# Optimization experiments

Hardware: AMD Instinct MI355X
Metric: run time of the kernel (lower is better)

## Reference

```python
import jax, jax.numpy as jnp
import numpy as np

THRESH = 0.95
SCALE = 20.0
KERNEL = 8  # feature_hw // proto_grid_size = 64 // 8
EPS = 1e-4


def _avg_pool(x, k):
    # x: [b, c, h, w] -> [b, c, h//k, w//k], non-overlapping k x k mean (AvgPool2d(k))
    b, c, h, w = x.shape
    return x.reshape(b, c, h // k, k, w // k, k).mean(axis=(3, 5))


def _safe_norm(x, eps=EPS):
    # L2-normalize along axis 1, clamping the norm at eps (matches safe_norm)
    n = jnp.sqrt(jnp.sum(x * x, axis=1, keepdims=True))
    return x / jnp.maximum(n, eps)


def setup_inputs() -> dict:
    key = jax.random.key(0)
    k1, k2, k3 = jax.random.split(key, 3)
    qry = jax.random.normal(k1, (32, 256, 64, 64), dtype=jnp.float32)
    sup_x = jax.random.normal(k2, (4, 256, 64, 64), dtype=jnp.float32)
    # binary support mask so that (sup_y > 0.95) selects the ones and pooled
    # occupancy exceeds 0.5 for ~half the grid cells -> valid prototypes exist
    sup_y = jax.random.randint(k3, (4, 1, 64, 64), 0, 2).astype(jnp.float32)
    return {"qry": qry, "sup_x": sup_x, "sup_y": sup_y}


def reference(qry, sup_x, sup_y):
    # ---- normalize query features (gridconv mode) ----
    qn = _safe_norm(qry)                                  # [B, C, H, W]

    # ---- prototype extraction (gridconv) ----
    mask_bin = (sup_y > THRESH).astype(qry.dtype)         # [bs, 1, H, W]
    feat_pooled = _avg_pool(sup_x, KERNEL)                # [bs, C, G, G]
    mask_pooled = _avg_pool(mask_bin, KERNEL)             # [bs, 1, G, G]
    valid = (mask_pooled[:, 0] > 0.5).reshape(-1)         # [P] with P = bs*G*G

    C = feat_pooled.shape[1]
    # gather all pooled locations in (image, hi, wi) order, mask out invalid ones
    protos = jnp.transpose(feat_pooled, (0, 2, 3, 1)).reshape(-1, C)  # [P, C]
    protos_n = _safe_norm(protos)                         # [P, C]

    # ---- prediction: conv2d with 1x1 prototype kernels == channel contraction ----
    dists = jnp.einsum('bchw,pc->bphw', qn, protos_n) * SCALE  # [B, P, H, W]
    vmask = valid[None, :, None, None]
    logits = jnp.where(vmask, dists, -jnp.inf)
    w = jax.nn.softmax(logits, axis=1)                    # invalid protos get 0 weight
    pred = jnp.sum(w * jnp.where(vmask, dists, 0.0), axis=1, keepdims=True)  # [B,1,H,W]

    debug_assign = jnp.argmax(logits, axis=1).astype(dists.dtype)  # [B, H, W]
    proto_grid = mask_bin                                 # (sup_y > thresh).float()
    return (pred, debug_assign, proto_grid)
```

## Files before the change

### kernel.cpp

```cpp
#include <hip/hip_runtime.h>
#include <math.h>

constexpr int BQ = 32;
constexpr int C  = 256;
constexpr int HW = 4096;
constexpr int W  = 64;
constexpr int P  = 256;
constexpr float THRESH = 0.95f;
constexpr float SCALE  = 20.0f;
constexpr float EPSF   = 1e-4f;
constexpr double EPSD  = 1e-4;
constexpr float GAP_THRESH = 2e-3f;
constexpr int MAXSUS = 65536;

constexpr int OUT_ASSIGN = BQ * HW;
constexpr int OUT_GRID   = 2 * BQ * HW;

typedef __attribute__((ext_vector_type(8))) short short8;
typedef __attribute__((ext_vector_type(4))) float floatx4;

static __device__ __forceinline__ unsigned short f2bf(float x) {
    unsigned u = __float_as_uint(x);
    u += 0x7FFFu + ((u >> 16) & 1u);
    return (unsigned short)(u >> 16);
}
static __device__ __forceinline__ float bf2f(unsigned short h) {
    return __uint_as_float(((unsigned)h) << 16);
}

#define FRAGOFF(tile, ks, h, lane) (((((tile) * 8 + (ks)) * 2 + (h)) * 64 + (lane)) * 8)

static __device__ __forceinline__ void gl_lds16(const unsigned short* gp, unsigned short* lp) {
    __builtin_amdgcn_global_load_lds(
        (const __attribute__((address_space(1))) unsigned int*)gp,
        (__attribute__((address_space(3))) unsigned int*)lp, 16, 0, 0);
}

__global__ __launch_bounds__(256)
void prep_kernel(const float* __restrict__ sup_x, const float* __restrict__ sup_y,
                 float* __restrict__ out, unsigned short* __restrict__ pB,
                 double* __restrict__ pn64, int* __restrict__ valid,
                 int* __restrict__ counter)
{
    const int p = blockIdx.x;
    const int t = threadIdx.x;
    const int s = p >> 6, gy = (p >> 3) & 7, gx = p & 7;

    const float* base = sup_x + ((size_t)(s * C + t)) * HW + (gy * 8) * W + gx * 8;
    double sum = 0.0;
#pragma unroll
    for (int r = 0; r < 8; ++r) {
        const float4 a  = *(const float4*)(base + r * W);
        const float4 bq = *(const float4*)(base + r * W + 4);
        sum += (double)a.x;  sum += (double)a.y;  sum += (double)a.z;  sum += (double)a.w;
        sum += (double)bq.x; sum += (double)bq.y; sum += (double)bq.z; sum += (double)bq.w;
    }
    const double mean = sum * (1.0 / 64.0);

    __shared__ double red[256];
    red[t] = mean * mean;
    __syncthreads();
    for (int off = 128; off > 0; off >>= 1) {
        if (t < off) red[t] += red[t + off];
        __syncthreads();
    }
    const double nrm = sqrt(red[0]);
    const double pnv = mean / fmax(nrm, EPSD);
    pn64[(size_t)p * C + t] = pnv;

    const float pnf = (float)pnv;
    const unsigned short phi = f2bf(pnf);
    const unsigned short plo = f2bf(pnf - bf2f(phi));
    const int nt = p >> 4, ks = t >> 5, lane = (((t >> 3) & 3) << 4) | (p & 15), j = t & 7;
    pB[FRAGOFF(nt, ks, 0, lane) + j] = phi;
    pB[FRAGOFF(nt, ks, 1, lane) + j] = plo;

    bool mybit = false;
    if (t < 64) {
        const int r = t >> 3, k = t & 7;
        mybit = sup_y[s * HW + (gy * 8 + r) * W + gx * 8 + k] > THRESH;
    }
    const unsigned long long bm = __ballot(mybit);
    if (t == 0) {
        valid[p] = (__popcll(bm) > 32) ? 1 : 0;
        if (p == 0) *counter = 0;
    }
    if (t < 64) {
        const int i = p * 64 + t;
        out[OUT_GRID + i] = (sup_y[i] > THRESH) ? 1.0f : 0.0f;
    }
}

__global__ __launch_bounds__(256, 4)
void dist_kernel(const float* __restrict__ qry, const unsigned short* __restrict__ pB,
                 const int* __restrict__ valid, float* __restrict__ out,
                 int* __restrict__ counter, int* __restrict__ suspects)
{
    __shared__ unsigned short ldsB[16 * 2 * 64 * 8];
    __shared__ int validLds[P];

    const int t    = threadIdx.x;
    const int w    = t >> 6;
    const int l    = t & 63;
    const int quad = l >> 4;
    const int m    = l & 15;

    const int b    = blockIdx.x >> 6;
    const int pos0 = (blockIdx.x & 63) * 64;

    validLds[t] = valid[t];

    const float* qp = qry + (size_t)b * C * HW + pos0 + w * 16 + m;

    floatx4 acc[16];
#pragma unroll
    for (int nt = 0; nt < 16; ++nt) acc[nt] = (floatx4){0.f, 0.f, 0.f, 0.f};

    float vbuf[8];
#pragma unroll
    for (int j = 0; j < 8; ++j)
        vbuf[j] = qp[(size_t)(quad * 8 + j) * HW];

    float ssq = 0.f;
#pragma unroll
    for (int ks = 0; ks < 8; ++ks) {
        __syncthreads();
#pragma unroll
        for (int i = 0; i < 8; ++i) {
            const int idx = w * 8 + i, nt = idx >> 1, h = idx & 1;
            gl_lds16(pB + FRAGOFF(nt, ks, h, 0) + l * 8,
                     &ldsB[(nt * 2 + h) * 512]);
        }
        short8 h8, l8;
#pragma unroll
        for (int j = 0; j < 8; ++j) {
            const float v = vbuf[j];
            ssq = fmaf(v, v, ssq);
            const unsigned short hi = f2bf(v);
            h8[j] = (short)hi;
            l8[j] = (short)f2bf(v - bf2f(hi));
        }
        if (ks < 7) {
#pragma unroll
            for (int j = 0; j < 8; ++j)
                vbuf[j] = qp[(size_t)((ks + 1) * 32 + quad * 8 + j) * HW];
        }
        __syncthreads();
#pragma unroll
        for (int nt = 0; nt < 16; ++nt) {
            const short8 bh = *(const short8*)&ldsB[((nt * 2 + 0) * 64 + l) * 8];
            const short8 bl = *(const short8*)&ldsB[((nt * 2 + 1) * 64 + l) * 8];
            acc[nt] = __builtin_amdgcn_mfma_f32_16x16x32_bf16(h8, bh, acc[nt], 0, 0, 0);
            acc[nt] = __builtin_amdgcn_mfma_f32_16x16x32_bf16(h8, bl, acc[nt], 0, 0, 0);
            acc[nt] = __builtin_amdgcn_mfma_f32_16x16x32_bf16(l8, bh, acc[nt], 0, 0, 0);
        }
    }

    ssq += __shfl_xor(ssq, 16);
    ssq += __shfl_xor(ssq, 32);
    const float scalev = SCALE / fmaxf(sqrtf(ssq), EPSF);

    int vbits = 0;
#pragma unroll
    for (int nt = 0; nt < 16; ++nt) vbits |= validLds[nt * 16 + m] << nt;

    float scr[4];
#pragma unroll
    for (int r = 0; r < 4; ++r) scr[r] = __shfl(scalev, quad * 4 + r);
#pragma unroll
    for (int nt = 0; nt < 16; ++nt)
#pragma unroll
        for (int r = 0; r < 4; ++r) acc[nt][r] *= scr[r];

#pragma unroll
    for (int r = 0; r < 4; ++r) {
        float m1 = -INFINITY, m2 = -INFINITY; int id = 0x7fffffff;
#pragma unroll
        for (int nt = 0; nt < 16; ++nt) {
            if (vbits & (1 << nt)) {
                const float d = acc[nt][r];
                if (d > m1)      { m2 = m1; m1 = d; id = nt * 16 + m; }
                else if (d > m2) { m2 = d; }
            }
        }
#pragma unroll
        for (int sh = 1; sh < 16; sh <<= 1) {
            const float om1 = __shfl_xor(m1, sh);
            const float om2 = __shfl_xor(m2, sh);
            const int   oid = __shfl_xor(id, sh);
            if (om1 > m1) { m2 = fmaxf(m1, om2); m1 = om1; id = oid; }
            else { if (om1 == m1 && oid < id) id = oid; m2 = fmaxf(m2, om1); }
        }
        const int posg = b * HW + pos0 + w * 16 + quad * 4 + r;
        if (m == 0) {
            out[OUT_ASSIGN + posg] = (float)id;
            if (m1 - m2 < GAP_THRESH) {
                const int slot = atomicAdd(counter, 1);
                if (slot < MAXSUS) suspects[slot] = posg;
            }
        }
        float se = 0.f, sw = 0.f;
#pragma unroll
        for (int nt = 0; nt < 16; ++nt) {
            if (vbits & (1 << nt)) {
                const float d = acc[nt][r];
                const float e = __expf(d - m1);
                se += e; sw = fmaf(e, d, sw);
            }
        }
#pragma unroll
        for (int sh = 1; sh < 16; sh <<= 1) {
            se += __shfl_xor(se, sh);
            sw += __shfl_xor(sw, sh);
        }
        if (m == 0) out[posg] = sw / se;
    }
}

__global__ __launch_bounds__(256)
void recheck_kernel(const float* __restrict__ qry, const double* __restrict__ pn64,
                    const int* __restrict__ valid, const int* __restrict__ counter,
                    const int* __restrict__ suspects, float* __restrict__ out)
{
    __shared__ float  qsh[16][256];
    __shared__ double pd[4];
    __shared__ int    pi[4];
    const int t = threadIdx.x;
    const int w = t >> 6, l = t & 63;
    int n = *counter; if (n > MAXSUS) n = MAXSUS;
    const int nb = (n + 15) >> 4;

    for (int batch = blockIdx.x; batch < nb; batch += gridDim.x) {
        const int base = batch * 16;
        const int cnt = (n - base < 16) ? (n - base) : 16;
        for (int s = 0; s < cnt; ++s) {
            const int pos = suspects[base + s];
            qsh[s][t] = qry[(size_t)(pos >> 12) * (C * HW) + (size_t)t * HW + (pos & (HW - 1))];
        }
        __syncthreads();

        double acc[16];
#pragma unroll
        for (int s = 0; s < 16; ++s) acc[s] = 0.0;
        const double* pr = pn64 + (size_t)t * C;
#pragma unroll 4
        for (int c = 0; c < C; ++c) {
            const double pv = pr[c];
#pragma unroll
            for (int s = 0; s < 16; ++s) acc[s] = fma((double)qsh[s][c], pv, acc[s]);
        }
        const bool vl = valid[t] != 0;
        for (int s = 0; s < cnt; ++s) {
            double dv = vl ? acc[s] : -INFINITY;
            int id = t;
#pragma unroll
            for (int sh = 1; sh < 64; sh <<= 1) {
                const double od = __shfl_xor(dv, sh);
                const int    oi = __shfl_xor(id, sh);
                if (od > dv || (od == dv && oi < id)) { dv = od; id = oi; }
            }
            if (l == 0) { pd[w] = dv; pi[w] = id; }
            __syncthreads();
            if (t == 0) {
                double bd = pd[0]; int bi = pi[0];
                for (int ww = 1; ww < 4; ++ww)
                    if (pd[ww] > bd || (pd[ww] == bd && pi[ww] < bi)) { bd = pd[ww]; bi = pi[ww]; }
                out[OUT_ASSIGN + suspects[base + s]] = (float)bi;
            }
            __syncthreads();
        }
    }
}

extern "C" void kernel_launch(void* const* d_in, const int* in_sizes, int n_in,
                              void* d_out, int out_size, void* d_ws, size_t ws_size,
                              hipStream_t stream)
{
    const float* qry   = (const float*)d_in[0];
    const float* sup_x = (const float*)d_in[1];
    const float* sup_y = (const float*)d_in[2];
    float* out = (float*)d_out;
    char*  ws  = (char*)d_ws;

    unsigned short* pB       = (unsigned short*)(ws);
    double*         pn64     = (double*)(ws + 256 * 1024);
    int*            valid    = (int*)(ws + 768 * 1024);
    int*            counter  = (int*)(ws + 768 * 1024 + 1024);
    int*            suspects = (int*)(ws + 768 * 1024 + 2048);

    prep_kernel<<<dim3(P), dim3(256), 0, stream>>>(sup_x, sup_y, out, pB, pn64, valid, counter);
    dist_kernel<<<dim3(BQ * (HW / 64)), dim3(256), 0, stream>>>(qry, pB, valid, out, counter, suspects);
    recheck_kernel<<<dim3(256), dim3(256), 0, stream>>>(qry, pn64, valid, counter, suspects, out);
}
```

Before: 292.2 us.

## Process two position tiles per wave to reuse LDS prototype fragments

```diff
diff --git a/kernel.cpp b/kernel.cpp
--- a/kernel.cpp
+++ b/kernel.cpp
@@ -91,7 +91,7 @@
     }
 }
 
-__global__ __launch_bounds__(256, 4)
+__global__ __launch_bounds__(256, 2)
 void dist_kernel(const float* __restrict__ qry, const unsigned short* __restrict__ pB,
                  const int* __restrict__ valid, float* __restrict__ out,
                  int* __restrict__ counter, int* __restrict__ suspects)
@@ -105,115 +105,135 @@
     const int quad = l >> 4;
     const int m    = l & 15;
 
-    const int b    = blockIdx.x >> 6;
-    const int pos0 = (blockIdx.x & 63) * 64;
+    const int b    = blockIdx.x >> 5;
+    const int pos0 = (blockIdx.x & 31) * 128;
 
     validLds[t] = valid[t];
 
-    const float* qp = qry + (size_t)b * C * HW + pos0 + w * 16 + m;
-
-    floatx4 acc[16];
-#pragma unroll
-    for (int nt = 0; nt < 16; ++nt) acc[nt] = (floatx4){0.f, 0.f, 0.f, 0.f};
-
-    float vbuf[8];
-#pragma unroll
-    for (int j = 0; j < 8; ++j)
-        vbuf[j] = qp[(size_t)(quad * 8 + j) * HW];
-
-    float ssq = 0.f;
+    const float* qp0 = qry + (size_t)b * C * HW + pos0 + w * 32 + m;
+    const float* qp1 = qp0 + 16;
+
+    floatx4 acc[2][16];
+#pragma unroll
+    for (int p2 = 0; p2 < 2; ++p2)
+#pragma unroll
+        for (int nt = 0; nt < 16; ++nt) acc[p2][nt] = (floatx4){0.f, 0.f, 0.f, 0.f};
+
+    float vbuf[2][2][8];
+#pragma unroll
+    for (int j = 0; j < 8; ++j) {
+        vbuf[0][0][j] = qp0[(size_t)(quad * 8 + j) * HW];
+        vbuf[0][1][j] = qp1[(size_t)(quad * 8 + j) * HW];
+    }
+
+    float ssq0 = 0.f, ssq1 = 0.f;
 #pragma unroll
     for (int ks = 0; ks < 8; ++ks) {
         __syncthreads();
+        if (ks < 7) {
+#pragma unroll
+            for (int j = 0; j < 8; ++j) {
+                vbuf[(ks + 1) & 1][0][j] = qp0[(size_t)((ks + 1) * 32 + quad * 8 + j) * HW];
+                vbuf[(ks + 1) & 1][1][j] = qp1[(size_t)((ks + 1) * 32 + quad * 8 + j) * HW];
+            }
+        }
 #pragma unroll
         for (int i = 0; i < 8; ++i) {
             const int idx = w * 8 + i, nt = idx >> 1, h = idx & 1;
             gl_lds16(pB + FRAGOFF(nt, ks, h, 0) + l * 8,
                      &ldsB[(nt * 2 + h) * 512]);
         }
-        short8 h8, l8;
+        short8 h80, l80, h81, l81;
 #pragma unroll
         for (int j = 0; j < 8; ++j) {
-            const float v = vbuf[j];
-            ssq = fmaf(v, v, ssq);
-            const unsigned short hi = f2bf(v);
-            h8[j] = (short)hi;
-            l8[j] = (short)f2bf(v - bf2f(hi));
-        }
-        if (ks < 7) {
-#pragma unroll
-            for (int j = 0; j < 8; ++j)
-                vbuf[j] = qp[(size_t)((ks + 1) * 32 + quad * 8 + j) * HW];
+            const float v0 = vbuf[ks & 1][0][j];
+            const float v1 = vbuf[ks & 1][1][j];
+            ssq0 = fmaf(v0, v0, ssq0);
+            ssq1 = fmaf(v1, v1, ssq1);
+            const unsigned short hi0 = f2bf(v0);
+            const unsigned short hi1 = f2bf(v1);
+            h80[j] = (short)hi0;  l80[j] = (short)f2bf(v0 - bf2f(hi0));
+            h81[j] = (short)hi1;  l81[j] = (short)f2bf(v1 - bf2f(hi1));
         }
         __syncthreads();
 #pragma unroll
         for (int nt = 0; nt < 16; ++nt) {
             const short8 bh = *(const short8*)&ldsB[((nt * 2 + 0) * 64 + l) * 8];
             const short8 bl = *(const short8*)&ldsB[((nt * 2 + 1) * 64 + l) * 8];
-            acc[nt] = __builtin_amdgcn_mfma_f32_16x16x32_bf16(h8, bh, acc[nt], 0, 0, 0);
-            acc[nt] = __builtin_amdgcn_mfma_f32_16x16x32_bf16(h8, bl, acc[nt], 0, 0, 0);
-            acc[nt] = __builtin_amdgcn_mfma_f32_16x16x32_bf16(l8, bh, acc[nt], 0, 0, 0);
-        }
-    }
-
-    ssq += __shfl_xor(ssq, 16);
-    ssq += __shfl_xor(ssq, 32);
-    const float scalev = SCALE / fmaxf(sqrtf(ssq), EPSF);
+            acc[0][nt] = __builtin_amdgcn_mfma_f32_16x16x32_bf16(h80, bh, acc[0][nt], 0, 0, 0);
+            acc[0][nt] = __builtin_amdgcn_mfma_f32_16x16x32_bf16(h80, bl, acc[0][nt], 0, 0, 0);
+            acc[0][nt] = __builtin_amdgcn_mfma_f32_16x16x32_bf16(l80, bh, acc[0][nt], 0, 0, 0);
+            acc[1][nt] = __builtin_amdgcn_mfma_f32_16x16x32_bf16(h81, bh, acc[1][nt], 0, 0, 0);
+            acc[1][nt] = __builtin_amdgcn_mfma_f32_16x16x32_bf16(h81, bl, acc[1][nt], 0, 0, 0);
+            acc[1][nt] = __builtin_amdgcn_mfma_f32_16x16x32_bf16(l81, bh, acc[1][nt], 0, 0, 0);
+        }
+    }
+
+    ssq0 += __shfl_xor(ssq0, 16);
+    ssq0 += __shfl_xor(ssq0, 32);
+    ssq1 += __shfl_xor(ssq1, 16);
+    ssq1 += __shfl_xor(ssq1, 32);
+    const float scale0 = SCALE / fmaxf(sqrtf(ssq0), EPSF);
+    const float scale1 = SCALE / fmaxf(sqrtf(ssq1), EPSF);
 
     int vbits = 0;
 #pragma unroll
     for (int nt = 0; nt < 16; ++nt) vbits |= validLds[nt * 16 + m] << nt;
 
-    float scr[4];
-#pragma unroll
-    for (int r = 0; r < 4; ++r) scr[r] = __shfl(scalev, quad * 4 + r);
-#pragma unroll
-    for (int nt = 0; nt < 16; ++nt)
-#pragma unroll
-        for (int r = 0; r < 4; ++r) acc[nt][r] *= scr[r];
-
-#pragma unroll
-    for (int r = 0; r < 4; ++r) {
-        float m1 = -INFINITY, m2 = -INFINITY; int id = 0x7fffffff;
-#pragma unroll
-        for (int nt = 0; nt < 16; ++nt) {
-            if (vbits & (1 << nt)) {
-                const float d = acc[nt][r];
-                if (d > m1)      { m2 = m1; m1 = d; id = nt * 16 + m; }
-                else if (d > m2) { m2 = d; }
-            }
-        }
-#pragma unroll
-        for (int sh = 1; sh < 16; sh <<= 1) {
-            const float om1 = __shfl_xor(m1, sh);
-            const float om2 = __shfl_xor(m2, sh);
-            const int   oid = __shfl_xor(id, sh);
-            if (om1 > m1) { m2 = fmaxf(m1, om2); m1 = om1; id = oid; }
-            else { if (om1 == m1 && oid < id) id = oid; m2 = fmaxf(m2, om1); }
-        }
-        const int posg = b * HW + pos0 + w * 16 + quad * 4 + r;
-        if (m == 0) {
-            out[OUT_ASSIGN + posg] = (float)id;
-            if (m1 - m2 < GAP_THRESH) {
-                const int slot = atomicAdd(counter, 1);
-                if (slot < MAXSUS) suspects[slot] = posg;
-            }
-        }
-        float se = 0.f, sw = 0.f;
-#pragma unroll
-        for (int nt = 0; nt < 16; ++nt) {
-            if (vbits & (1 << nt)) {
-                const float d = acc[nt][r];
-                const float e = __expf(d - m1);
-                se += e; sw = fmaf(e, d, sw);
-            }
-        }
-#pragma unroll
-        for (int sh = 1; sh < 16; sh <<= 1) {
-            se += __shfl_xor(se, sh);
-            sw += __shfl_xor(sw, sh);
-        }
-        if (m == 0) out[posg] = sw / se;
+#pragma unroll
+    for (int p2 = 0; p2 < 2; ++p2) {
+        const float scalev = (p2 == 0) ? scale0 : scale1;
+        float scr[4];
+#pragma unroll
+        for (int r = 0; r < 4; ++r) scr[r] = __shfl(scalev, quad * 4 + r);
+#pragma unroll
+        for (int nt = 0; nt < 16; ++nt)
+#pragma unroll
+            for (int r = 0; r < 4; ++r) acc[p2][nt][r] *= scr[r];
+
+#pragma unroll
+        for (int r = 0; r < 4; ++r) {
+            float m1 = -INFINITY, m2 = -INFINITY; int id = 0x7fffffff;
+#pragma unroll
+            for (int nt = 0; nt < 16; ++nt) {
+                if (vbits & (1 << nt)) {
+                    const float d = acc[p2][nt][r];
+                    if (d > m1)      { m2 = m1; m1 = d; id = nt * 16 + m; }
+                    else if (d > m2) { m2 = d; }
+                }
+            }
+#pragma unroll
+            for (int sh = 1; sh < 16; sh <<= 1) {
+                const float om1 = __shfl_xor(m1, sh);
+                const float om2 = __shfl_xor(m2, sh);
+                const int   oid = __shfl_xor(id, sh);
+                if (om1 > m1) { m2 = fmaxf(m1, om2); m1 = om1; id = oid; }
+                else { if (om1 == m1 && oid < id) id = oid; m2 = fmaxf(m2, om1); }
+            }
+            const int posg = b * HW + pos0 + w * 32 + p2 * 16 + quad * 4 + r;
+            if (m == 0) {
+                out[OUT_ASSIGN + posg] = (float)id;
+                if (m1 - m2 < GAP_THRESH) {
+                    const int slot = atomicAdd(counter, 1);
+                    if (slot < MAXSUS) suspects[slot] = posg;
+                }
+            }
+            float se = 0.f, sw = 0.f;
+#pragma unroll
+            for (int nt = 0; nt < 16; ++nt) {
+                if (vbits & (1 << nt)) {
+                    const float d = acc[p2][nt][r];
+                    const float e = __expf(d - m1);
+                    se += e; sw = fmaf(e, d, sw);
+                }
+            }
+#pragma unroll
+            for (int sh = 1; sh < 16; sh <<= 1) {
+                se += __shfl_xor(se, sh);
+                sw += __shfl_xor(sw, sh);
+            }
+            if (m == 0) out[posg] = sw / se;
+        }
     }
 }
 
@@ -289,6 +309,6 @@
     int*            suspects = (int*)(ws + 768 * 1024 + 2048);
 
     prep_kernel<<<dim3(P), dim3(256), 0, stream>>>(sup_x, sup_y, out, pB, pn64, valid, counter);
-    dist_kernel<<<dim3(BQ * (HW / 64)), dim3(256), 0, stream>>>(qry, pB, valid, out, counter, suspects);
+    dist_kernel<<<dim3(BQ * (HW / 128)), dim3(256), 0, stream>>>(qry, pB, valid, out, counter, suspects);
     recheck_kernel<<<dim3(256), dim3(256), 0, stream>>>(qry, pn64, valid, counter, suspects, out);
 }
```

Measured after the change: 302.3 us. 3.4% more time.

## Switch distance GEMM to 32x32 MFMA tiles with cross-wave softmax merge

Applied to the files above, without the earlier changes.

```diff
diff --git a/kernel.cpp b/kernel.cpp
--- a/kernel.cpp
+++ b/kernel.cpp
@@ -17,7 +17,7 @@
 constexpr int OUT_GRID   = 2 * BQ * HW;
 
 typedef __attribute__((ext_vector_type(8))) short short8;
-typedef __attribute__((ext_vector_type(4))) float floatx4;
+typedef __attribute__((ext_vector_type(16))) float floatx16;
 
 static __device__ __forceinline__ unsigned short f2bf(float x) {
     unsigned u = __float_as_uint(x);
@@ -28,7 +28,7 @@
     return __uint_as_float(((unsigned)h) << 16);
 }
 
-#define FRAGOFF(tile, ks, h, lane) (((((tile) * 8 + (ks)) * 2 + (h)) * 64 + (lane)) * 8)
+#define FRAGOFF32(pt, ks16, h, lane) (((((pt) * 16 + (ks16)) * 2 + (h)) * 64 + (lane)) * 8)
 
 static __device__ __forceinline__ void gl_lds16(const unsigned short* gp, unsigned short* lp) {
     __builtin_amdgcn_global_load_lds(
@@ -71,9 +71,9 @@
     const float pnf = (float)pnv;
     const unsigned short phi = f2bf(pnf);
     const unsigned short plo = f2bf(pnf - bf2f(phi));
-    const int nt = p >> 4, ks = t >> 5, lane = (((t >> 3) & 3) << 4) | (p & 15), j = t & 7;
-    pB[FRAGOFF(nt, ks, 0, lane) + j] = phi;
-    pB[FRAGOFF(nt, ks, 1, lane) + j] = plo;
+    const int pt = p >> 5, ks16 = t >> 4, lane = (((t >> 3) & 1) << 5) | (p & 31), j = t & 7;
+    pB[FRAGOFF32(pt, ks16, 0, lane) + j] = phi;
+    pB[FRAGOFF32(pt, ks16, 1, lane) + j] = plo;
 
     bool mybit = false;
     if (t < 64) {
@@ -96,30 +96,38 @@
                  const int* __restrict__ valid, float* __restrict__ out,
                  int* __restrict__ counter, int* __restrict__ suspects)
 {
-    __shared__ unsigned short ldsB[16 * 2 * 64 * 8];
+    __shared__ unsigned short ldsB[8 * 2 * 2 * 64 * 8];
     __shared__ int validLds[P];
-
-    const int t    = threadIdx.x;
-    const int w    = t >> 6;
-    const int l    = t & 63;
-    const int quad = l >> 4;
-    const int m    = l & 15;
+    __shared__ float part_m1[2][64], part_m2[2][64], part_se[2][64], part_sw[2][64];
+    __shared__ int   part_id[2][64];
+
+    const int t  = threadIdx.x;
+    const int w  = t >> 6;
+    const int l  = t & 63;
+    const int lr = l & 31;
+    const int lh = l >> 5;
+    const int wp = w >> 1;
+    const int wn = w & 1;
 
     const int b    = blockIdx.x >> 6;
     const int pos0 = (blockIdx.x & 63) * 64;
 
     validLds[t] = valid[t];
 
-    const float* qp = qry + (size_t)b * C * HW + pos0 + w * 16 + m;
-
-    floatx4 acc[16];
-#pragma unroll
-    for (int nt = 0; nt < 16; ++nt) acc[nt] = (floatx4){0.f, 0.f, 0.f, 0.f};
-
-    float vbuf[8];
-#pragma unroll
-    for (int j = 0; j < 8; ++j)
-        vbuf[j] = qp[(size_t)(quad * 8 + j) * HW];
+    const float* qp = qry + (size_t)b * C * HW + pos0 + wp * 32 + lr;
+
+    floatx16 acc[4];
+#pragma unroll
+    for (int nt = 0; nt < 4; ++nt)
+#pragma unroll
+        for (int r = 0; r < 16; ++r) acc[nt][r] = 0.f;
+
+    float vbuf[2][8];
+#pragma unroll
+    for (int hf = 0; hf < 2; ++hf)
+#pragma unroll
+        for (int j = 0; j < 8; ++j)
+            vbuf[hf][j] = qp[(size_t)(hf * 16 + lh * 8 + j) * HW];
 
     float ssq = 0.f;
 #pragma unroll
@@ -127,81 +135,81 @@
         __syncthreads();
 #pragma unroll
         for (int i = 0; i < 8; ++i) {
-            const int idx = w * 8 + i, nt = idx >> 1, h = idx & 1;
-            gl_lds16(pB + FRAGOFF(nt, ks, h, 0) + l * 8,
-                     &ldsB[(nt * 2 + h) * 512]);
-        }
-        short8 h8, l8;
-#pragma unroll
-        for (int j = 0; j < 8; ++j) {
-            const float v = vbuf[j];
-            ssq = fmaf(v, v, ssq);
-            const unsigned short hi = f2bf(v);
-            h8[j] = (short)hi;
-            l8[j] = (short)f2bf(v - bf2f(hi));
-        }
+            const int c = w * 8 + i, pt = c >> 2, hf = (c >> 1) & 1, h = c & 1;
+            gl_lds16(pB + FRAGOFF32(pt, ks * 2 + hf, h, 0) + l * 8,
+                     &ldsB[c * 512]);
+        }
+        short8 ah[2], al[2];
+#pragma unroll
+        for (int hf = 0; hf < 2; ++hf)
+#pragma unroll
+            for (int j = 0; j < 8; ++j) {
+                const float v = vbuf[hf][j];
+                ssq = fmaf(v, v, ssq);
+                const unsigned short hi = f2bf(v);
+                ah[hf][j] = (short)hi;
+                al[hf][j] = (short)f2bf(v - bf2f(hi));
+            }
         if (ks < 7) {
 #pragma unroll
-            for (int j = 0; j < 8; ++j)
-                vbuf[j] = qp[(size_t)((ks + 1) * 32 + quad * 8 + j) * HW];
+            for (int hf = 0; hf < 2; ++hf)
+#pragma unroll
+                for (int j = 0; j < 8; ++j)
+                    vbuf[hf][j] = qp[(size_t)((ks + 1) * 32 + hf * 16 + lh * 8 + j) * HW];
         }
         __syncthreads();
 #pragma unroll
-        for (int nt = 0; nt < 16; ++nt) {
-            const short8 bh = *(const short8*)&ldsB[((nt * 2 + 0) * 64 + l) * 8];
-            const short8 bl = *(const short8*)&ldsB[((nt * 2 + 1) * 64 + l) * 8];
-            acc[nt] = __builtin_amdgcn_mfma_f32_16x16x32_bf16(h8, bh, acc[nt], 0, 0, 0);
-            acc[nt] = __builtin_amdgcn_mfma_f32_16x16x32_bf16(h8, bl, acc[nt], 0, 0, 0);
-            acc[nt] = __builtin_amdgcn_mfma_f32_16x16x32_bf16(l8, bh, acc[nt], 0, 0, 0);
-        }
-    }
-
-    ssq += __shfl_xor(ssq, 16);
+        for (int nt = 0; nt < 4; ++nt) {
+            const int g = wn * 4 + nt;
+#pragma unroll
+            for (int hf = 0; hf < 2; ++hf) {
+                const short8 bh = *(const short8*)&ldsB[((g * 2 + hf) * 2 + 0) * 512 + l * 8];
+                const short8 bl = *(const short8*)&ldsB[((g * 2 + hf) * 2 + 1) * 512 + l * 8];
+                acc[nt] = __builtin_amdgcn_mfma_f32_32x32x16_bf16(ah[hf], bh, acc[nt], 0, 0, 0);
+                acc[nt] = __builtin_amdgcn_mfma_f32_32x32x16_bf16(ah[hf], bl, acc[nt], 0, 0, 0);
+                acc[nt] = __builtin_amdgcn_mfma_f32_32x32x16_bf16(al[hf], bh, acc[nt], 0, 0, 0);
+            }
+        }
+    }
+
     ssq += __shfl_xor(ssq, 32);
     const float scalev = SCALE / fmaxf(sqrtf(ssq), EPSF);
 
     int vbits = 0;
 #pragma unroll
-    for (int nt = 0; nt < 16; ++nt) vbits |= validLds[nt * 16 + m] << nt;
-
-    float scr[4];
-#pragma unroll
-    for (int r = 0; r < 4; ++r) scr[r] = __shfl(scalev, quad * 4 + r);
-#pragma unroll
-    for (int nt = 0; nt < 16; ++nt)
-#pragma unroll
-        for (int r = 0; r < 4; ++r) acc[nt][r] *= scr[r];
-
-#pragma unroll
-    for (int r = 0; r < 4; ++r) {
+    for (int nt = 0; nt < 4; ++nt) vbits |= validLds[(wn * 4 + nt) * 32 + lr] << nt;
+
+    float scr[16];
+#pragma unroll
+    for (int r = 0; r < 16; ++r)
+        scr[r] = __shfl(scalev, 4 * lh + (r & 3) + 8 * (r >> 2));
+#pragma unroll
+    for (int nt = 0; nt < 4; ++nt)
+#pragma unroll
+        for (int r = 0; r < 16; ++r) acc[nt][r] *= scr[r];
+
+#pragma unroll
+    for (int r = 0; r < 16; ++r) {
         float m1 = -INFINITY, m2 = -INFINITY; int id = 0x7fffffff;
 #pragma unroll
-        for (int nt = 0; nt < 16; ++nt) {
+        for (int nt = 0; nt < 4; ++nt) {
             if (vbits & (1 << nt)) {
                 const float d = acc[nt][r];
-                if (d > m1)      { m2 = m1; m1 = d; id = nt * 16 + m; }
+                if (d > m1)      { m2 = m1; m1 = d; id = (wn * 4 + nt) * 32 + lr; }
                 else if (d > m2) { m2 = d; }
             }
         }
 #pragma unroll
-        for (int sh = 1; sh < 16; sh <<= 1) {
+        for (int sh = 1; sh < 32; sh <<= 1) {
             const float om1 = __shfl_xor(m1, sh);
             const float om2 = __shfl_xor(m2, sh);
             const int   oid = __shfl_xor(id, sh);
             if (om1 > m1) { m2 = fmaxf(m1, om2); m1 = om1; id = oid; }
             else { if (om1 == m1 && oid < id) id = oid; m2 = fmaxf(m2, om1); }
         }
-        const int posg = b * HW + pos0 + w * 16 + quad * 4 + r;
-        if (m == 0) {
-            out[OUT_ASSIGN + posg] = (float)id;
-            if (m1 - m2 < GAP_THRESH) {
-                const int slot = atomicAdd(counter, 1);
-                if (slot < MAXSUS) suspects[slot] = posg;
-            }
-        }
         float se = 0.f, sw = 0.f;
 #pragma unroll
-        for (int nt = 0; nt < 16; ++nt) {
+        for (int nt = 0; nt < 4; ++nt) {
             if (vbits & (1 << nt)) {
                 const float d = acc[nt][r];
                 const float e = __expf(d - m1);
@@ -209,11 +217,36 @@
             }
         }
 #pragma unroll
-        for (int sh = 1; sh < 16; sh <<= 1) {
+        for (int sh = 1; sh < 32; sh <<= 1) {
             se += __shfl_xor(se, sh);
             sw += __shfl_xor(sw, sh);
         }
-        if (m == 0) out[posg] = sw / se;
+        if (lr == 0) {
+            const int pidx = wp * 32 + 4 * lh + (r & 3) + 8 * (r >> 2);
+            part_m1[wn][pidx] = m1;
+            part_m2[wn][pidx] = m2;
+            part_id[wn][pidx] = id;
+            part_se[wn][pidx] = se;
+            part_sw[wn][pidx] = sw;
+        }
+    }
+    __syncthreads();
+
+    if (t < 64) {
+        const float m1a = part_m1[0][t], m1b = part_m1[1][t];
+        float M, m2g; int id;
+        if (m1a >= m1b) { M = m1a; id = part_id[0][t]; m2g = fmaxf(part_m2[0][t], m1b); }
+        else            { M = m1b; id = part_id[1][t]; m2g = fmaxf(part_m2[1][t], m1a); }
+        const float ea = __expf(m1a - M), eb = __expf(m1b - M);
+        const float se = part_se[0][t] * ea + part_se[1][t] * eb;
+        const float sw = part_sw[0][t] * ea + part_sw[1][t] * eb;
+        const int posg = b * HW + pos0 + t;
+        out[OUT_ASSIGN + posg] = (float)id;
+        if (M - m2g < GAP_THRESH) {
+            const int slot = atomicAdd(counter, 1);
+            if (slot < MAXSUS) suspects[slot] = posg;
+        }
+        out[posg] = sw / se;
     }
 }
 
```

Measured after the change: 396.9 us. +35.8%, slower.

## Assign one suspect per wavefront in FP64 argmax recheck kernel

Applied to the files above, without the earlier changes.

```diff
diff --git a/kernel.cpp b/kernel.cpp
--- a/kernel.cpp
+++ b/kernel.cpp
@@ -222,53 +222,53 @@
                     const int* __restrict__ valid, const int* __restrict__ counter,
                     const int* __restrict__ suspects, float* __restrict__ out)
 {
-    __shared__ float  qsh[16][256];
-    __shared__ double pd[4];
-    __shared__ int    pi[4];
+    __shared__ float qsh[4][256];
     const int t = threadIdx.x;
     const int w = t >> 6, l = t & 63;
     int n = *counter; if (n > MAXSUS) n = MAXSUS;
-    const int nb = (n + 15) >> 4;
+    const int nb = (n + 3) >> 2;
 
     for (int batch = blockIdx.x; batch < nb; batch += gridDim.x) {
-        const int base = batch * 16;
-        const int cnt = (n - base < 16) ? (n - base) : 16;
-        for (int s = 0; s < cnt; ++s) {
-            const int pos = suspects[base + s];
-            qsh[s][t] = qry[(size_t)(pos >> 12) * (C * HW) + (size_t)t * HW + (pos & (HW - 1))];
-        }
-        __syncthreads();
-
-        double acc[16];
-#pragma unroll
-        for (int s = 0; s < 16; ++s) acc[s] = 0.0;
-        const double* pr = pn64 + (size_t)t * C;
+        const int si = batch * 4 + w;
+        const bool active = si < n;
+        int pos = 0;
+        if (active) {
+            pos = suspects[si];
+#pragma unroll
+            for (int k = 0; k < 4; ++k) {
+                const int c = l + 64 * k;
+                qsh[w][c] = qry[(size_t)(pos >> 12) * (C * HW) + (size_t)c * HW + (pos & (HW - 1))];
+            }
+        }
+        __syncthreads();
+        if (active) {
+            double best = -INFINITY; int bid = 0x7fffffff;
+#pragma unroll
+            for (int k = 0; k < 4; ++k) {
+                const int p = l + 64 * k;
+                if (valid[p]) {
+                    const double* pr = pn64 + (size_t)p * C;
+                    double a0 = 0.0, a1 = 0.0, a2 = 0.0, a3 = 0.0;
 #pragma unroll 4
-        for (int c = 0; c < C; ++c) {
-            const double pv = pr[c];
-#pragma unroll
-            for (int s = 0; s < 16; ++s) acc[s] = fma((double)qsh[s][c], pv, acc[s]);
-        }
-        const bool vl = valid[t] != 0;
-        for (int s = 0; s < cnt; ++s) {
-            double dv = vl ? acc[s] : -INFINITY;
-            int id = t;
+                    for (int c = 0; c < C; c += 4) {
+                        a0 = fma((double)qsh[w][c + 0], pr[c + 0], a0);
+                        a1 = fma((double)qsh[w][c + 1], pr[c + 1], a1);
+                        a2 = fma((double)qsh[w][c + 2], pr[c + 2], a2);
+                        a3 = fma((double)qsh[w][c + 3], pr[c + 3], a3);
+                    }
+                    const double d = (a0 + a1) + (a2 + a3);
+                    if (d > best) { best = d; bid = p; }
+                }
+            }
 #pragma unroll
             for (int sh = 1; sh < 64; sh <<= 1) {
-                const double od = __shfl_xor(dv, sh);
-                const int    oi = __shfl_xor(id, sh);
-                if (od > dv || (od == dv && oi < id)) { dv = od; id = oi; }
-            }
-            if (l == 0) { pd[w] = dv; pi[w] = id; }
-            __syncthreads();
-            if (t == 0) {
-                double bd = pd[0]; int bi = pi[0];
-                for (int ww = 1; ww < 4; ++ww)
-                    if (pd[ww] > bd || (pd[ww] == bd && pi[ww] < bi)) { bd = pd[ww]; bi = pi[ww]; }
-                out[OUT_ASSIGN + suspects[base + s]] = (float)bi;
-            }
-            __syncthreads();
-        }
+                const double od = __shfl_xor(best, sh);
+                const int    oi = __shfl_xor(bid, sh);
+                if (od > best || (od == best && oi < bid)) { best = od; bid = oi; }
+            }
+            if (l == 0) out[OUT_ASSIGN + pos] = (float)bid;
+        }
+        __syncthreads();
     }
 }
 
@@ -290,5 +290,5 @@
 
     prep_kernel<<<dim3(P), dim3(256), 0, stream>>>(sup_x, sup_y, out, pB, pn64, valid, counter);
     dist_kernel<<<dim3(BQ * (HW / 64)), dim3(256), 0, stream>>>(qry, pB, valid, out, counter, suspects);
-    recheck_kernel<<<dim3(256), dim3(256), 0, stream>>>(qry, pn64, valid, counter, suspects, out);
-}
+    recheck_kernel<<<dim3(1024), dim3(256), 0, stream>>>(qry, pn64, valid, counter, suspects, out);
+}
```

After: 274.7 us (median of 2 runs). 6.0% less time.
